# Kernel tuning notes

Measured on AMD Instinct MI355X. Metric: run time of the kernel, lower is better.

## Reference

```python
import jax, jax.numpy as jnp
import numpy as np

HIDDEN = 4096
N_HEADS = 32
N_KV_HEADS = 8
HEAD_DIM = HIDDEN // N_HEADS
KV_GROUPS = N_HEADS // N_KV_HEADS
TEMPERATURE = 1.0
NEG_INF = -1e9


def _bitlinear(x, W):
    """BitNet b1.58 BitLinear: per-token int8 activation quant + ternary weight quant (quant-dequant)."""
    # activation: absmax int8 per last dim
    a_scale = 127.0 / jnp.clip(jnp.max(jnp.abs(x), axis=-1, keepdims=True), 1e-5, None)
    xq = jnp.clip(jnp.round(x * a_scale), -128.0, 127.0) / a_scale
    # weight: ternary with mean-abs scale
    w_scale = jnp.clip(jnp.mean(jnp.abs(W)), 1e-5, None)
    Wq = jnp.clip(jnp.round(W / w_scale), -1.0, 1.0) * w_scale
    return jnp.einsum('bsh,oh->bso', xq, Wq)


def _base2_softmax(x, temperature=TEMPERATURE):
    # numerically stable 2^x softmax: 2^((x-m)/T) / sum
    m = jnp.max(x, axis=-1, keepdims=True)
    p = jnp.exp2((x - m) / temperature)
    return p / jnp.sum(p, axis=-1, keepdims=True)


def setup_inputs() -> dict:
    key = jax.random.key(0)
    ks = jax.random.split(key, 6)
    B, S = 2, 2048
    hidden_states = jax.random.normal(ks[0], (B, S, HIDDEN), dtype=jnp.float32)
    # additive causal mask [B, 1, S, S]
    causal = jnp.tril(jnp.ones((S, S), dtype=bool))
    attention_mask = jnp.where(causal, 0.0, NEG_INF).astype(jnp.float32)[None, None]
    attention_mask = jnp.broadcast_to(attention_mask, (B, 1, S, S))
    Wq = jax.random.normal(ks[1], (HIDDEN, HIDDEN), dtype=jnp.float32) * 0.02
    Wk = jax.random.normal(ks[2], (N_KV_HEADS * HEAD_DIM, HIDDEN), dtype=jnp.float32) * 0.02
    Wv = jax.random.normal(ks[3], (N_KV_HEADS * HEAD_DIM, HIDDEN), dtype=jnp.float32) * 0.02
    Wo = jax.random.normal(ks[4], (HIDDEN, HIDDEN), dtype=jnp.float32) * 0.02
    return {"hidden_states": hidden_states, "attention_mask": attention_mask,
            "Wq": Wq, "Wk": Wk, "Wv": Wv, "Wo": Wo}


def reference(hidden_states, attention_mask, Wq, Wk, Wv, Wo):
    B, S, _ = hidden_states.shape
    q = _bitlinear(hidden_states, Wq).reshape(B, S, N_HEADS, HEAD_DIM).transpose(0, 2, 1, 3)
    k = _bitlinear(hidden_states, Wk).reshape(B, S, N_KV_HEADS, HEAD_DIM).transpose(0, 2, 1, 3)
    v = _bitlinear(hidden_states, Wv).reshape(B, S, N_KV_HEADS, HEAD_DIM).transpose(0, 2, 1, 3)
    # GQA: repeat each kv head KV_GROUPS times along head dim
    k = jnp.repeat(k, KV_GROUPS, axis=1)
    v = jnp.repeat(v, KV_GROUPS, axis=1)
    attn_weights = jnp.einsum('bhqd,bhkd->bhqk', q, k) / np.sqrt(HEAD_DIM).astype(np.float32)
    attn_weights = attn_weights + attention_mask
    attn_weights = _base2_softmax(attn_weights)
    attn_output = jnp.einsum('bhqk,bhkd->bhqd', attn_weights, v)
    attn_output = attn_output.transpose(0, 2, 1, 3).reshape(B, S, HIDDEN)
    return _bitlinear(attn_output, Wo)
```

## Files before the change

### kernel.cpp

```cpp
#include <hip/hip_runtime.h>
#include <stdint.h>


typedef float  f32x4 __attribute__((ext_vector_type(4)));
typedef short  s16x8 __attribute__((ext_vector_type(8)));
typedef int    i32x4 __attribute__((ext_vector_type(4)));

__device__ __forceinline__ uint16_t f2b(float f) {
  uint32_t u = __float_as_uint(f);
  return (uint16_t)((u + 0x7FFFu + ((u >> 16) & 1u)) >> 16);
}
__device__ __forceinline__ uint32_t cvt_pk_bf16(float lo, float hi) {
  uint32_t r;
  asm("v_cvt_pk_bf16_f32 %0, %1, %2" : "=v"(r) : "v"(lo), "v"(hi));
  return r;
}
__device__ __forceinline__ void gl_lds16(const void* g, void* l) {
  __builtin_amdgcn_global_load_lds((const __attribute__((address_space(1))) unsigned int*)g,
                                   (__attribute__((address_space(3))) unsigned int*)l, 16, 0, 0);
}
__device__ __forceinline__ f32x4 mfma_bf16(s16x8 a, s16x8 b, f32x4 c) {
  return __builtin_amdgcn_mfma_f32_16x16x32_bf16(a, b, c, 0, 0, 0);
}
__device__ __forceinline__ i32x4 mfma_i8(i32x4 a, i32x4 b, i32x4 c) {
  return __builtin_amdgcn_mfma_i32_16x16x64_i8(a, b, c, 0, 0, 0);
}

__global__ __launch_bounds__(256) void k_qact_f32(const float* __restrict__ x,
                                                  int8_t* __restrict__ xq, float* __restrict__ rs) {
  __shared__ float red[4];
  const int row = blockIdx.x, t = threadIdx.x;
  const float4* xr = (const float4*)(x + (size_t)row * 4096);
  float v[16];
  #pragma unroll
  for (int i = 0; i < 4; i++) {
    float4 f = xr[t + 256 * i];
    v[i*4+0] = f.x; v[i*4+1] = f.y; v[i*4+2] = f.z; v[i*4+3] = f.w;
  }
  float mx = 0.f;
  #pragma unroll
  for (int i = 0; i < 16; i++) mx = fmaxf(mx, fabsf(v[i]));
  for (int o = 1; o < 64; o <<= 1) mx = fmaxf(mx, __shfl_xor(mx, o));
  if ((t & 63) == 0) red[t >> 6] = mx;
  __syncthreads();
  mx = fmaxf(fmaxf(red[0], red[1]), fmaxf(red[2], red[3]));
  mx = fmaxf(mx, 1e-5f);
  const float a = 127.f / mx;
  if (t == 0) rs[row] = mx * (1.f / 127.f);
  uint32_t* dst = (uint32_t*)(xq + (size_t)row * 4096);
  #pragma unroll
  for (int i = 0; i < 4; i++) {
    uint32_t w = 0;
    #pragma unroll
    for (int j = 0; j < 4; j++) {
      float q = rintf(v[i*4+j] * a);
      q = fmaxf(-128.f, fminf(127.f, q));
      w |= ((uint32_t)((int)q & 255)) << (j * 8);
    }
    dst[t + 256 * i] = w;
  }
}

__global__ __launch_bounds__(256) void k_abssum_part(const float* __restrict__ wq, const float* __restrict__ wk,
                                                     const float* __restrict__ wv, const float* __restrict__ wo,
                                                     double* __restrict__ part) {
  __shared__ double red[4];
  const int blk = blockIdx.x, t = threadIdx.x;
  const float* src; size_t base;
  if (blk < 1024)      { src = wq; base = (size_t)blk * 16384; }
  else if (blk < 1280) { src = wk; base = (size_t)(blk - 1024) * 16384; }
  else if (blk < 1536) { src = wv; base = (size_t)(blk - 1280) * 16384; }
  else                 { src = wo; base = (size_t)(blk - 1536) * 16384; }
  double s = 0.0;
  #pragma unroll
  for (int r = 0; r < 16; r++) {
    float4 f = *(const float4*)(src + base + r * 1024 + t * 4);
    s += (double)fabsf(f.x) + (double)fabsf(f.y) + (double)fabsf(f.z) + (double)fabsf(f.w);
  }
  for (int o = 1; o < 64; o <<= 1) s += __shfl_xor(s, o);
  if ((t & 63) == 0) red[t >> 6] = s;
  __syncthreads();
  if (t == 0) part[blk] = red[0] + red[1] + red[2] + red[3];
}

__global__ __launch_bounds__(256) void k_reduce_sums(const double* __restrict__ part, double* __restrict__ sums) {
  const int w = threadIdx.x >> 6, lane = threadIdx.x & 63;
  const int s0 = (w == 0) ? 0 : (w == 1) ? 1024 : (w == 2) ? 1280 : 1536;
  const int s1 = (w == 0) ? 1024 : (w == 1) ? 1280 : (w == 2) ? 1536 : 2560;
  double s = 0.0;
  for (int i = s0 + lane; i < s1; i += 64) s += part[i];
  for (int o = 1; o < 64; o <<= 1) s += __shfl_xor(s, o);
  if (lane == 0) sums[w] = s;
}

__global__ __launch_bounds__(256) void k_quant_w_all(const float* __restrict__ wq, const float* __restrict__ wk,
                                                     const float* __restrict__ wv, const float* __restrict__ wo,
                                                     int8_t* __restrict__ wqkv, int8_t* __restrict__ woq,
                                                     const double* __restrict__ sums) {
  const int blk = blockIdx.x, t = threadIdx.x;
  const float* src; int8_t* dst; size_t base; int sidx; double ivn;
  if (blk < 1024)      { src = wq; dst = wqkv;                        base = (size_t)blk * 16384;          sidx = 0; ivn = 1.0 / 16777216.0; }
  else if (blk < 1280) { src = wk; dst = wqkv + (size_t)4096 * 4096;  base = (size_t)(blk - 1024) * 16384; sidx = 1; ivn = 1.0 / 4194304.0;  }
  else if (blk < 1536) { src = wv; dst = wqkv + (size_t)5120 * 4096;  base = (size_t)(blk - 1280) * 16384; sidx = 2; ivn = 1.0 / 4194304.0;  }
  else                 { src = wo; dst = woq;                         base = (size_t)(blk - 1536) * 16384; sidx = 3; ivn = 1.0 / 16777216.0; }
  const float ws = (float)fmax(sums[sidx] * ivn, 1e-5);
  #pragma unroll
  for (int r = 0; r < 16; r++) {
    size_t e = base + r * 1024 + t * 4;
    float4 f = *(const float4*)(src + e);
    float hv[4] = {f.x, f.y, f.z, f.w};
    uint32_t w = 0;
    #pragma unroll
    for (int j = 0; j < 4; j++) {
      float q = rintf(hv[j] / ws);
      q = fmaxf(-1.f, fminf(1.f, q));
      w |= ((uint32_t)((int)q & 255)) << (j * 8);
    }
    *(uint32_t*)(dst + e) = w;
  }
}

template<int MODE>
__global__ __launch_bounds__(256) void k_gemm_i8(const int8_t* __restrict__ A, const int8_t* __restrict__ Bw,
                                                 const float* __restrict__ rs, const double* __restrict__ sums,
                                                 uint16_t* __restrict__ qb, uint16_t* __restrict__ kb,
                                                 uint16_t* __restrict__ vb, float* __restrict__ outp) {
  __shared__ int8_t lA[16384];
  __shared__ int8_t lB[16384];
  const int bn = blockIdx.x, bm = blockIdx.y;
  const int t = threadIdx.x, wave = t >> 6, lane = t & 63;
  const int quad = lane >> 4, l15 = lane & 15;
  const int wm = wave >> 1, wn = wave & 1;

  i32x4 acc[4][4];
  #pragma unroll
  for (int i = 0; i < 4; i++)
    #pragma unroll
    for (int j = 0; j < 4; j++) acc[i][j] = (i32x4){0, 0, 0, 0};

  const size_t arow0 = (size_t)bm * 128;
  const size_t brow0 = (size_t)bn * 128;

  for (int k0 = 0; k0 < 4096; k0 += 128) {
    #pragma unroll
    for (int r = 0; r < 4; r++) {
      int off = r * 4096 + wave * 1024 + lane * 16;
      int row = off >> 7;
      int pos = (off >> 4) & 7;
      int chunk = pos ^ (row & 7);
      gl_lds16(A  + (arow0 + row) * 4096 + k0 + chunk * 16, lA + r * 4096 + wave * 1024);
      gl_lds16(Bw + (brow0 + row) * 4096 + k0 + chunk * 16, lB + r * 4096 + wave * 1024);
    }
    __syncthreads();
    #pragma unroll
    for (int ks = 0; ks < 2; ks++) {
      i32x4 af[4], bf[4];
      #pragma unroll
      for (int i = 0; i < 4; i++) {
        int m = wm * 64 + i * 16 + l15;
        int c = ks * 4 + quad;
        af[i] = *(const i32x4*)(lA + m * 128 + (c ^ (m & 7)) * 16);
        int n = wn * 64 + i * 16 + l15;
        bf[i] = *(const i32x4*)(lB + n * 128 + (c ^ (n & 7)) * 16);
      }
      #pragma unroll
      for (int i = 0; i < 4; i++)
        #pragma unroll
        for (int j = 0; j < 4; j++)
          acc[i][j] = mfma_i8(af[i], bf[j], acc[i][j]);
    }
    __syncthreads();
  }

  float wsc; int sel = 0;
  if (MODE == 0) {
    if (bn < 32)      { wsc = (float)fmax(sums[0] * (1.0 / 16777216.0), 1e-5); sel = 0; }
    else if (bn < 40) { wsc = (float)fmax(sums[1] * (1.0 / 4194304.0),  1e-5); sel = 1; }
    else              { wsc = (float)fmax(sums[2] * (1.0 / 4194304.0),  1e-5); sel = 2; }
  } else {
    wsc = (float)fmax(sums[3] * (1.0 / 16777216.0), 1e-5);
  }
  #pragma unroll
  for (int i = 0; i < 4; i++) {
    #pragma unroll
    for (int r = 0; r < 4; r++) {
      int token = bm * 128 + wm * 64 + i * 16 + quad * 4 + r;
      float rv = rs[token] * wsc;
      #pragma unroll
      for (int j = 0; j < 4; j++) {
        int o = bn * 128 + wn * 64 + j * 16 + l15;
        float val = (float)acc[i][j][r] * rv;
        if (MODE == 0) {
          int b = token >> 11, s2 = token & 2047;
          if (sel == 0) {
            int hh = o >> 7, d = o & 127;
            qb[(((size_t)b * 32 + hh) * 2048 + s2) * 128 + d] = f2b(val * 0.08838834764831845f);
          } else if (sel == 1) {
            int o2 = o - 4096; int g = o2 >> 7, d = o2 & 127;
            kb[(((size_t)b * 8 + g) * 2048 + s2) * 128 + d] = f2b(val);
          } else {
            int o2 = o - 5120; int g = o2 >> 7, d = o2 & 127;
            vb[(((size_t)b * 8 + g) * 2048 + s2) * 128 + d] = f2b(val);
          }
        } else {
          outp[(size_t)token * 4096 + o] = val;
        }
      }
    }
  }
}

__global__ __launch_bounds__(256) void k_transpose_v(const uint16_t* __restrict__ v, uint16_t* __restrict__ vt) {
  __shared__ uint16_t tile[64][72];
  const int bs = blockIdx.x * 64, bd = blockIdx.y * 64, g = blockIdx.z;
  const int t = threadIdx.x;
  const uint16_t* src = v + ((size_t)g * 2048 + bs) * 128 + bd;
  #pragma unroll
  for (int it = 0; it < 2; it++) {
    int r = (t >> 3) + it * 32;
    int c = (t & 7) * 8;
    uint4 u = *(const uint4*)(src + (size_t)r * 128 + c);
    uint16_t* p = &tile[r][c];
    p[0] = u.x & 0xffff; p[1] = u.x >> 16; p[2] = u.y & 0xffff; p[3] = u.y >> 16;
    p[4] = u.z & 0xffff; p[5] = u.z >> 16; p[6] = u.w & 0xffff; p[7] = u.w >> 16;
  }
  __syncthreads();
  uint16_t* dst = vt + ((size_t)g * 128 + bd) * 2048 + bs;
  #pragma unroll
  for (int it = 0; it < 2; it++) {
    int r = (t >> 3) + it * 32;
    int c = (t & 7) * 8;
    uint32_t w0 = tile[c+0][r] | ((uint32_t)tile[c+1][r] << 16);
    uint32_t w1 = tile[c+2][r] | ((uint32_t)tile[c+3][r] << 16);
    uint32_t w2 = tile[c+4][r] | ((uint32_t)tile[c+5][r] << 16);
    uint32_t w3 = tile[c+6][r] | ((uint32_t)tile[c+7][r] << 16);
    *(uint4*)(dst + (size_t)r * 2048 + c) = make_uint4(w0, w1, w2, w3);
  }
}

__global__ __launch_bounds__(256, 2) void k_attn(const uint16_t* __restrict__ qg, const uint16_t* __restrict__ kg,
                                                 const uint16_t* __restrict__ vtg, float* __restrict__ attn) {
  __shared__ char smem[32768];
  const int p = blockIdx.x, bh = blockIdx.y;
  const int b = bh >> 5, h = bh & 31, kv = h >> 2;
  const int t = threadIdx.x, wave = t >> 6, lane = t & 63;
  const int quad = lane >> 4, l15 = lane & 15;

  const char* qbase = (const char*)(qg + (((size_t)b * 32 + h) * 2048) * 128);
  const char* ksrc  = (const char*)(kg + (((size_t)b * 8 + kv) * 2048) * 128);
  const char* vsrc  = (const char*)(vtg + (((size_t)b * 8 + kv) * 128) * 2048);

  for (int pass = 0; pass < 2; pass++) {
    const int qt = pass ? (15 - p) : p;

    __syncthreads();
    #pragma unroll
    for (int r = 0; r < 8; r++) {
      int off = r * 4096 + t * 16;
      int row = off >> 8, pos = (off >> 4) & 15;
      int chunk = pos ^ (row & 7);
      gl_lds16(qbase + (size_t)(qt * 128 + row) * 256 + chunk * 16, smem + off);
    }
    __syncthreads();
    s16x8 qf[2][4];
    #pragma unroll
    for (int hh = 0; hh < 2; hh++)
      #pragma unroll
      for (int ks = 0; ks < 4; ks++) {
        int n = hh * 64 + wave * 16 + l15;
        int c = ks * 4 + quad;
        qf[hh][ks] = *(const s16x8*)(smem + n * 256 + ((c ^ (n & 7))) * 16);
      }

    float Mx[2] = {-3.0e38f, -3.0e38f};
    float Ls[2] = {0.f, 0.f};
    f32x4 Ov[2][8];
    #pragma unroll
    for (int hh = 0; hh < 2; hh++)
      #pragma unroll
      for (int mf = 0; mf < 8; mf++) Ov[hh][mf] = (f32x4){0, 0, 0, 0};

    const int nkt = 2 * qt + 1;
    for (int kt = 0; kt <= nkt; kt++) {
      __syncthreads();
      #pragma unroll
      for (int r = 0; r < 4; r++) {
        int off = r * 4096 + t * 16;
        { int row = off >> 8, pos = (off >> 4) & 15, chunk = pos ^ (row & 7);
          gl_lds16(ksrc + (size_t)(kt * 64 + row) * 256 + chunk * 16, smem + off); }
        { int row = off >> 7, pos = (off >> 4) & 7, chunk = pos ^ (row & 7);
          gl_lds16(vsrc + (size_t)row * 4096 + kt * 128 + chunk * 16, smem + 16384 + off); }
      }
      __syncthreads();

      f32x4 sc[2][4];
      #pragma unroll
      for (int hh = 0; hh < 2; hh++)
        #pragma unroll
        for (int mf = 0; mf < 4; mf++) sc[hh][mf] = (f32x4){0, 0, 0, 0};
      __builtin_amdgcn_s_setprio(1);
      #pragma unroll
      for (int ks = 0; ks < 4; ks++) {
        #pragma unroll
        for (int mf = 0; mf < 4; mf++) {
          int m = mf * 16 + l15;
          int c = ks * 4 + quad;
          s16x8 kf = *(const s16x8*)(smem + m * 256 + ((c ^ (m & 7))) * 16);
          sc[0][mf] = mfma_bf16(kf, qf[0][ks], sc[0][mf]);
          sc[1][mf] = mfma_bf16(kf, qf[1][ks], sc[1][mf]);
        }
      }
      __builtin_amdgcn_s_setprio(0);

      #pragma unroll
      for (int hh = 0; hh < 2; hh++) {
        if (kt >= 2 * qt + hh) {
          int qloc = hh * 64 + wave * 16 + l15;
          int kb = (kt - 2 * qt) * 64;
          #pragma unroll
          for (int mf = 0; mf < 4; mf++)
            #pragma unroll
            for (int r = 0; r < 4; r++) {
              int kloc = kb + mf * 16 + quad * 4 + r;
              if (kloc > qloc) sc[hh][mf][r] = -3.0e38f;
            }
        }
      }

      #pragma unroll
      for (int hh = 0; hh < 2; hh++) {
        float x = sc[hh][0][0];
        #pragma unroll
        for (int mf = 0; mf < 4; mf++)
          #pragma unroll
          for (int r = 0; r < 4; r++) x = fmaxf(x, sc[hh][mf][r]);
        x = fmaxf(x, __shfl_xor(x, 16));
        x = fmaxf(x, __shfl_xor(x, 32));
        if (!__all(x - Mx[hh] <= 8.f)) {
          float m2 = fmaxf(Mx[hh], x);
          float al = exp2f(Mx[hh] - m2);
          Mx[hh] = m2;
          Ls[hh] *= al;
          #pragma unroll
          for (int mf = 0; mf < 8; mf++)
            #pragma unroll
            for (int r = 0; r < 4; r++) Ov[hh][mf][r] *= al;
        }
        float s = 0.f;
        #pragma unroll
        for (int mf = 0; mf < 4; mf++)
          #pragma unroll
          for (int r = 0; r < 4; r++) {
            float pv = exp2f(sc[hh][mf][r] - Mx[hh]);
            sc[hh][mf][r] = pv;
            s += pv;
          }
        s += __shfl_xor(s, 16);
        s += __shfl_xor(s, 32);
        Ls[hh] += s;
      }

      #pragma unroll
      for (int ks = 0; ks < 2; ks++) {
        uint32_t pfw[2][4];
        #pragma unroll
        for (int hh = 0; hh < 2; hh++) {
          uint32_t pk[2][2];
          #pragma unroll
          for (int mfp = 0; mfp < 2; mfp++)
            #pragma unroll
            for (int pr = 0; pr < 2; pr++)
              pk[mfp][pr] = cvt_pk_bf16(sc[hh][2*ks+mfp][2*pr], sc[hh][2*ks+mfp][2*pr+1]);
          #pragma unroll
          for (int j2 = 0; j2 < 4; j2++) {
            int srcLane = ((quad & 1) * 2 + (j2 >> 1)) * 16 + l15;
            uint32_t a0 = __shfl(pk[0][j2 & 1], srcLane);
            uint32_t a1 = __shfl(pk[1][j2 & 1], srcLane);
            pfw[hh][j2] = (quad >= 2) ? a1 : a0;
          }
        }
        s16x8 pfr0 = *(const s16x8*)&pfw[0][0];
        s16x8 pfr1 = *(const s16x8*)&pfw[1][0];
        __builtin_amdgcn_s_setprio(1);
        #pragma unroll
        for (int mf = 0; mf < 8; mf++) {
          int m = mf * 16 + l15;
          int c = ks * 4 + quad;
          s16x8 vf = *(const s16x8*)(smem + 16384 + m * 128 + ((c ^ (m & 7))) * 16);
          Ov[0][mf] = mfma_bf16(vf, pfr0, Ov[0][mf]);
          Ov[1][mf] = mfma_bf16(vf, pfr1, Ov[1][mf]);
        }
        __builtin_amdgcn_s_setprio(0);
      }
    }

    #pragma unroll
    for (int hh = 0; hh < 2; hh++) {
      float inv = 1.f / Ls[hh];
      size_t token = (size_t)b * 2048 + qt * 128 + hh * 64 + wave * 16 + l15;
      float* obase = attn + token * 4096 + h * 128 + quad * 4;
      #pragma unroll
      for (int mf = 0; mf < 8; mf++) {
        float4 v4 = make_float4(Ov[hh][mf][0] * inv, Ov[hh][mf][1] * inv,
                                Ov[hh][mf][2] * inv, Ov[hh][mf][3] * inv);
        *(float4*)(obase + mf * 16) = v4;
      }
    }
  }
}

extern "C" void kernel_launch(void* const* d_in, const int* in_sizes, int n_in,
                              void* d_out, int out_size, void* d_ws, size_t ws_size,
                              hipStream_t stream) {
  (void)in_sizes; (void)out_size;
  if (n_in < 6) return;
  const float* hs = (const float*)d_in[0];
  const float* Wq = (const float*)d_in[2];
  const float* Wk = (const float*)d_in[3];
  const float* Wv = (const float*)d_in[4];
  const float* Wo = (const float*)d_in[5];
  float* out = (float*)d_out;

  char* p = (char*)d_ws;
  size_t off = 0;
  auto take = [&](size_t bytes) { char* r = p + off; off += (bytes + 255) & ~(size_t)255; return r; };
  int8_t*   xq1  = (int8_t*)  take((size_t)4096 * 4096);
  float*    rs1  = (float*)   take(4096 * 4);
  int8_t*   wqkv = (int8_t*)  take((size_t)6144 * 4096);
  int8_t*   woq  = (int8_t*)  take((size_t)4096 * 4096);
  uint16_t* qb   = (uint16_t*)take((size_t)2 * 32 * 2048 * 128 * 2);
  uint16_t* kb   = (uint16_t*)take((size_t)2 * 8 * 2048 * 128 * 2);
  uint16_t* vb   = (uint16_t*)take((size_t)2 * 8 * 2048 * 128 * 2);
  uint16_t* vtb  = (uint16_t*)take((size_t)2 * 8 * 2048 * 128 * 2);
  float*    attn = (float*)   take((size_t)4096 * 4096 * 4);
  int8_t*   xq2  = (int8_t*)  take((size_t)4096 * 4096);
  float*    rs2  = (float*)   take(4096 * 4);
  double*   part = (double*)  take(2560 * 8);
  double*   sums = (double*)  take(256);
  if (off > ws_size) return;

  k_abssum_part<<<2560, 256, 0, stream>>>(Wq, Wk, Wv, Wo, part);
  k_reduce_sums<<<1, 256, 0, stream>>>(part, sums);
  k_quant_w_all<<<2560, 256, 0, stream>>>(Wq, Wk, Wv, Wo, wqkv, woq, sums);
  k_qact_f32<<<4096, 256, 0, stream>>>(hs, xq1, rs1);
  k_gemm_i8<0><<<dim3(48, 32), 256, 0, stream>>>(xq1, wqkv, rs1, sums, qb, kb, vb, (float*)nullptr);
  k_transpose_v<<<dim3(32, 2, 16), 256, 0, stream>>>(vb, vtb);
  k_attn<<<dim3(8, 64), 256, 0, stream>>>(qb, kb, vtb, attn);
  k_qact_f32<<<4096, 256, 0, stream>>>(attn, xq2, rs2);
  k_gemm_i8<1><<<dim3(32, 32), 256, 0, stream>>>(xq2, woq, rs2, sums,
                                                 (uint16_t*)nullptr, (uint16_t*)nullptr, (uint16_t*)nullptr, out);
}
```

Measured before the change: 655.9 us.

## Double-buffer int8 GEMM with 256x256 tiles and 8-wave ping-pong schedule

Reworks the int8 MFMA GEMM from 128x128 tiles with 4 waves and a single LDS buffer into 256x256 tiles with 8 waves and double-buffered LDS. Global-to-LDS loads for the next K step are issued between the two MFMA halves, and barriers plus setprio are used to overlap memory with compute. The aim is more data reuse per tile and hiding of load latency. In exchange it uses more registers (32 accumulators per wave) and 64KB of LDS, and the grids shrink to 384 and 256 blocks, which may underfill the GPU.

```diff
diff --git a/kernel.cpp b/kernel.cpp
--- a/kernel.cpp
+++ b/kernel.cpp
@@ -121,74 +121,117 @@
 }
 
 template<int MODE>
-__global__ __launch_bounds__(256) void k_gemm_i8(const int8_t* __restrict__ A, const int8_t* __restrict__ Bw,
-                                                 const float* __restrict__ rs, const double* __restrict__ sums,
-                                                 uint16_t* __restrict__ qb, uint16_t* __restrict__ kb,
-                                                 uint16_t* __restrict__ vb, float* __restrict__ outp) {
-  __shared__ int8_t lA[16384];
-  __shared__ int8_t lB[16384];
+__global__ __launch_bounds__(512, 2) void k_gemm_i8(const int8_t* __restrict__ A, const int8_t* __restrict__ Bw,
+                                                    const float* __restrict__ rs, const double* __restrict__ sums,
+                                                    uint16_t* __restrict__ qb, uint16_t* __restrict__ kb,
+                                                    uint16_t* __restrict__ vb, float* __restrict__ outp) {
+  __shared__ int8_t lA[2][16384];
+  __shared__ int8_t lB[2][16384];
   const int bn = blockIdx.x, bm = blockIdx.y;
   const int t = threadIdx.x, wave = t >> 6, lane = t & 63;
   const int quad = lane >> 4, l15 = lane & 15;
-  const int wm = wave >> 1, wn = wave & 1;
-
-  i32x4 acc[4][4];
-  #pragma unroll
-  for (int i = 0; i < 4; i++)
+  const int wm = wave >> 2, wn = wave & 3;
+
+  i32x4 acc[8][4];
+  #pragma unroll
+  for (int i = 0; i < 8; i++)
     #pragma unroll
     for (int j = 0; j < 4; j++) acc[i][j] = (i32x4){0, 0, 0, 0};
 
-  const size_t arow0 = (size_t)bm * 128;
-  const size_t brow0 = (size_t)bn * 128;
-
-  for (int k0 = 0; k0 < 4096; k0 += 128) {
-    #pragma unroll
-    for (int r = 0; r < 4; r++) {
-      int off = r * 4096 + wave * 1024 + lane * 16;
-      int row = off >> 7;
-      int pos = (off >> 4) & 7;
-      int chunk = pos ^ (row & 7);
-      gl_lds16(A  + (arow0 + row) * 4096 + k0 + chunk * 16, lA + r * 4096 + wave * 1024);
-      gl_lds16(Bw + (brow0 + row) * 4096 + k0 + chunk * 16, lB + r * 4096 + wave * 1024);
-    }
-    __syncthreads();
-    #pragma unroll
-    for (int ks = 0; ks < 2; ks++) {
-      i32x4 af[4], bf[4];
-      #pragma unroll
-      for (int i = 0; i < 4; i++) {
-        int m = wm * 64 + i * 16 + l15;
-        int c = ks * 4 + quad;
-        af[i] = *(const i32x4*)(lA + m * 128 + (c ^ (m & 7)) * 16);
-        int n = wn * 64 + i * 16 + l15;
-        bf[i] = *(const i32x4*)(lB + n * 128 + (c ^ (n & 7)) * 16);
-      }
-      #pragma unroll
-      for (int i = 0; i < 4; i++)
-        #pragma unroll
-        for (int j = 0; j < 4; j++)
-          acc[i][j] = mfma_i8(af[i], bf[j], acc[i][j]);
-    }
-    __syncthreads();
+  const size_t arow0 = (size_t)bm * 256;
+  const size_t brow0 = (size_t)bn * 256;
+
+  auto stageA = [&](int buf, int k0) {
+    #pragma unroll
+    for (int r = 0; r < 2; r++) {
+      int off = r * 8192 + t * 16;
+      int s = off >> 7, p = (off >> 4) & 7;
+      int e = p ^ (s & 7);
+      int grow = 2 * s + (e >> 2);
+      gl_lds16(A + (arow0 + grow) * 4096 + k0 + (e & 3) * 16, &lA[buf][off]);
+    }
+  };
+  auto stageB = [&](int buf, int k0) {
+    #pragma unroll
+    for (int r = 0; r < 2; r++) {
+      int off = r * 8192 + t * 16;
+      int s = off >> 7, p = (off >> 4) & 7;
+      int e = p ^ (s & 7);
+      int grow = 2 * s + (e >> 2);
+      gl_lds16(Bw + (brow0 + grow) * 4096 + k0 + (e & 3) * 16, &lB[buf][off]);
+    }
+  };
+  auto rdoff = [&](int m) {
+    int s = m >> 1;
+    int p = (((m & 1) << 2) | quad) ^ (s & 7);
+    return s * 128 + p * 16;
+  };
+
+  stageA(0, 0); stageB(0, 0);
+  asm volatile("s_waitcnt vmcnt(0)" ::: "memory");
+  __builtin_amdgcn_s_barrier();
+
+  for (int kt = 0; kt < 64; kt++) {
+    const int cur = kt & 1;
+    const int8_t* la = lA[cur];
+    const int8_t* lb = lB[cur];
+    const int k0n = (kt + 1) * 64;
+
+    i32x4 af0[4], bf[4];
+    #pragma unroll
+    for (int i = 0; i < 4; i++) {
+      af0[i] = *(const i32x4*)(la + rdoff(wm * 128 + i * 16 + l15));
+      bf[i]  = *(const i32x4*)(lb + rdoff(wn * 64 + i * 16 + l15));
+    }
+    if (kt < 63) stageA(cur ^ 1, k0n);
+    __builtin_amdgcn_s_barrier();
+    asm volatile("s_waitcnt lgkmcnt(0)" ::: "memory");
+    __builtin_amdgcn_sched_barrier(0);
+    __builtin_amdgcn_s_setprio(1);
+    #pragma unroll
+    for (int i = 0; i < 4; i++)
+      #pragma unroll
+      for (int j = 0; j < 4; j++)
+        acc[i][j] = mfma_i8(af0[i], bf[j], acc[i][j]);
+    __builtin_amdgcn_s_setprio(0);
+    __builtin_amdgcn_s_barrier();
+
+    i32x4 af1[4];
+    #pragma unroll
+    for (int i = 0; i < 4; i++)
+      af1[i] = *(const i32x4*)(la + rdoff(wm * 128 + 64 + i * 16 + l15));
+    if (kt < 63) stageB(cur ^ 1, k0n);
+    __builtin_amdgcn_s_barrier();
+    asm volatile("s_waitcnt lgkmcnt(0)" ::: "memory");
+    __builtin_amdgcn_sched_barrier(0);
+    __builtin_amdgcn_s_setprio(1);
+    #pragma unroll
+    for (int i = 0; i < 4; i++)
+      #pragma unroll
+      for (int j = 0; j < 4; j++)
+        acc[4 + i][j] = mfma_i8(af1[i], bf[j], acc[4 + i][j]);
+    __builtin_amdgcn_s_setprio(0);
+    asm volatile("s_waitcnt vmcnt(0)" ::: "memory");
+    __builtin_amdgcn_s_barrier();
   }
 
   float wsc; int sel = 0;
   if (MODE == 0) {
-    if (bn < 32)      { wsc = (float)fmax(sums[0] * (1.0 / 16777216.0), 1e-5); sel = 0; }
-    else if (bn < 40) { wsc = (float)fmax(sums[1] * (1.0 / 4194304.0),  1e-5); sel = 1; }
+    if (bn < 16)      { wsc = (float)fmax(sums[0] * (1.0 / 16777216.0), 1e-5); sel = 0; }
+    else if (bn < 20) { wsc = (float)fmax(sums[1] * (1.0 / 4194304.0),  1e-5); sel = 1; }
     else              { wsc = (float)fmax(sums[2] * (1.0 / 4194304.0),  1e-5); sel = 2; }
   } else {
     wsc = (float)fmax(sums[3] * (1.0 / 16777216.0), 1e-5);
   }
   #pragma unroll
-  for (int i = 0; i < 4; i++) {
+  for (int i = 0; i < 8; i++) {
     #pragma unroll
     for (int r = 0; r < 4; r++) {
-      int token = bm * 128 + wm * 64 + i * 16 + quad * 4 + r;
+      int token = bm * 256 + wm * 128 + (i >> 2) * 64 + (i & 3) * 16 + quad * 4 + r;
       float rv = rs[token] * wsc;
       #pragma unroll
       for (int j = 0; j < 4; j++) {
-        int o = bn * 128 + wn * 64 + j * 16 + l15;
+        int o = bn * 256 + wn * 64 + j * 16 + l15;
         float val = (float)acc[i][j][r] * rv;
         if (MODE == 0) {
           int b = token >> 11, s2 = token & 2047;
@@ -443,10 +486,10 @@
   k_reduce_sums<<<1, 256, 0, stream>>>(part, sums);
   k_quant_w_all<<<2560, 256, 0, stream>>>(Wq, Wk, Wv, Wo, wqkv, woq, sums);
   k_qact_f32<<<4096, 256, 0, stream>>>(hs, xq1, rs1);
-  k_gemm_i8<0><<<dim3(48, 32), 256, 0, stream>>>(xq1, wqkv, rs1, sums, qb, kb, vb, (float*)nullptr);
+  k_gemm_i8<0><<<dim3(24, 16), 512, 0, stream>>>(xq1, wqkv, rs1, sums, qb, kb, vb, (float*)nullptr);
   k_transpose_v<<<dim3(32, 2, 16), 256, 0, stream>>>(vb, vtb);
   k_attn<<<dim3(8, 64), 256, 0, stream>>>(qb, kb, vtb, attn);
   k_qact_f32<<<4096, 256, 0, stream>>>(attn, xq2, rs2);
-  k_gemm_i8<1><<<dim3(32, 32), 256, 0, stream>>>(xq2, woq, rs2, sums,
+  k_gemm_i8<1><<<dim3(16, 16), 512, 0, stream>>>(xq2, woq, rs2, sums,
                                                  (uint16_t*)nullptr, (uint16_t*)nullptr, (uint16_t*)nullptr, out);
 }
```

Measured after the change: 695.6 us. +6.1%, slower.
